# Performance work log

Measured on AMD Instinct MI355X. Metric: run time of the kernel, lower is better.

## Reference

```python
import jax, jax.numpy as jnp
import numpy as np

B, N, D, H, S = 2, 1024, 1024, 16, 4
DH = D // H  # dim_head = 64


def setup_inputs() -> dict:
    key = jax.random.key(0)
    ks = jax.random.split(key, 7)
    w = lambda k, shape: jax.random.normal(k, shape, dtype=jnp.float32) * 0.02
    return {
        "x": jax.random.normal(ks[0], (B, N, D), dtype=jnp.float32),
        "Wq": w(ks[1], (S, D, D)),
        "Wk": w(ks[2], (S, D, D)),
        "Wv": w(ks[3], (S, D, D)),
        "Wg": w(ks[4], (S, D)),
        "bg": jnp.zeros((S,), jnp.float32),
        "Wo": w(ks[5], (D, D)),
        "bo": jnp.zeros((D,), jnp.float32),
        "hyp_w": jnp.ones((S,), jnp.float32),
        "temperature": jnp.float32(1.0),
    }


def reference(x, Wq, Wk, Wv, Wg, bg, Wo, bo, hyp_w, temperature):
    # Training branch of EnhancedUncertaintyAttention, all S samples batched.
    b, n, d = x.shape
    scale = DH ** -0.5
    temp = jnp.clip(temperature, 0.1, 10.0)

    # coherence gate on mean-pooled tokens: [b, S]
    coh = jax.nn.sigmoid(x.mean(axis=1) @ Wg.T + bg)

    def proj(W):  # torch Linear: x @ W.T ; W: [S, out, in] -> [s,b,h,n,dh]
        y = jnp.einsum('bnd,sed->sbne', x, W)
        return y.reshape(S, b, n, H, DH).transpose(0, 1, 3, 2, 4)

    q, k, v = proj(Wq), proj(Wk), proj(Wv)

    dots = jnp.einsum('sbhid,sbhjd->sbhij', q, k) * scale
    attn = jax.nn.softmax(dots / temp, axis=-1)            # [S,b,h,n,n]
    out = jnp.einsum('sbhij,sbhjd->sbhid', attn, v)        # [S,b,h,n,dh]
    out = out.transpose(0, 1, 3, 2, 4).reshape(S, b, n, d) # [S,b,n,d]
    out = out * coh.T[:, :, None, None]                    # per-sample gate

    gw = jax.nn.softmax(hyp_w / temp)                      # hypothesis weights [S]
    combined = jnp.einsum('s,sbnd->bnd', gw, out)
    combined_attn = jnp.einsum('s,sbhij->bhij', gw, attn)

    y = combined @ Wo.T + bo  # to_out; dropout p treated as 0 (deterministic)
    return y, combined_attn.mean(axis=1)
```

## Files before the change

kernel.cpp:

```cpp
#include <hip/hip_runtime.h>
#include <hip/hip_bf16.h>

typedef __attribute__((ext_vector_type(8))) short s16x8;
typedef __attribute__((ext_vector_type(4))) float f32x4;

#define MAT2M 2097152
#define PPAD 72

__device__ __forceinline__ unsigned short f2bf(float f) {
  union { float f; unsigned u; } c; c.f = f;
  unsigned u = c.u;
  unsigned r = (u + 0x7fffu + ((u >> 16) & 1u)) >> 16;
  return (unsigned short)r;
}

__device__ __forceinline__ unsigned pk2bf(float a, float b) {
  union { __hip_bfloat162 h; unsigned u; } c;
  c.h = __float22bfloat162_rn(make_float2(a, b));
  return c.u;
}

__device__ __forceinline__ float bf2f(unsigned short u) {
  union { unsigned u; float f; } c; c.u = ((unsigned)u) << 16; return c.f;
}

__device__ __forceinline__ void async16(const unsigned short* g, unsigned short* l) {
  __builtin_amdgcn_global_load_lds(
      (const __attribute__((address_space(1))) unsigned int*)g,
      (__attribute__((address_space(3))) unsigned int*)l, 16, 0, 0);
}

__device__ __forceinline__ void stage64sw(const unsigned short* __restrict__ g,
                                          unsigned short* l, int wid, int ln) {
  const int rr = ln >> 3;
  const int gcol = ((ln & 7) ^ (rr & 7)) * 8;
#pragma unroll
  for (int c = 0; c < 2; ++c) {
    int r = (c * 4 + wid) * 8 + rr;
    async16(&g[(size_t)r * 1024 + gcol], &l[(c * 4 + wid) * 512 + ln * 8]);
  }
}

__global__ __launch_bounds__(256) void k_cvt(const float* __restrict__ in,
                                             unsigned short* __restrict__ out, int n) {
  int i = (blockIdx.x * 256 + threadIdx.x) * 4;
  if (i < n) {
    float4 v = *(const float4*)&in[i];
    ushort4 o;
    o.x = f2bf(v.x); o.y = f2bf(v.y); o.z = f2bf(v.z); o.w = f2bf(v.w);
    *(ushort4*)&out[i] = o;
  }
}

__global__ __launch_bounds__(256) void k_cvt3(const float* __restrict__ a,
                                              const float* __restrict__ b,
                                              const float* __restrict__ c,
                                              unsigned short* __restrict__ oa,
                                              unsigned short* __restrict__ ob,
                                              unsigned short* __restrict__ oc) {
  const float* in = blockIdx.y == 0 ? a : (blockIdx.y == 1 ? b : c);
  unsigned short* out = blockIdx.y == 0 ? oa : (blockIdx.y == 1 ? ob : oc);
  int i = (blockIdx.x * 256 + threadIdx.x) * 4;
  float4 v = *(const float4*)&in[i];
  ushort4 o;
  o.x = f2bf(v.x); o.y = f2bf(v.y); o.z = f2bf(v.z); o.w = f2bf(v.w);
  *(ushort4*)&out[i] = o;
}

__global__ __launch_bounds__(256) void k_meanx(const float* __restrict__ x,
                                               float* __restrict__ meanx) {
  int col = blockIdx.x * 256 + threadIdx.x;
  int b = col >> 10, d = col & 1023;
  int n0 = blockIdx.y * 64;
  float s = 0.f;
  for (int n = 0; n < 64; ++n)
    s += x[(size_t)b * 1048576 + (size_t)(n0 + n) * 1024 + d];
  atomicAdd(&meanx[col], s * (1.f / 1024.f));
}

__global__ __launch_bounds__(256) void k_prep(const float* __restrict__ meanx,
                                              const float* __restrict__ Wg,
                                              const float* __restrict__ bg,
                                              const float* __restrict__ hyp,
                                              const float* __restrict__ temp_p,
                                              float* __restrict__ prep) {
  int tid = threadIdx.x;
  int p = tid >> 5, c = tid & 31;
  int s = p >> 1, b = p & 1;
  float partial = 0.f;
  for (int d = c; d < 1024; d += 32)
    partial += meanx[b * 1024 + d] * Wg[s * 1024 + d];
#pragma unroll
  for (int m = 16; m >= 1; m >>= 1) partial += __shfl_xor(partial, m, 64);
  if (c == 0) {
    float coh = 1.f / (1.f + __expf(-(partial + bg[s])));
    prep[4 + s * 2 + b] = coh;
  }
  if (tid == 0) {
    float t = temp_p[0];
    t = fminf(fmaxf(t, 0.1f), 10.f);
    float it = 1.f / t;
    float e0 = hyp[0] * it, e1 = hyp[1] * it, e2 = hyp[2] * it, e3 = hyp[3] * it;
    float mx = fmaxf(fmaxf(e0, e1), fmaxf(e2, e3));
    float x0 = __expf(e0 - mx), x1 = __expf(e1 - mx), x2 = __expf(e2 - mx), x3 = __expf(e3 - mx);
    float inv = 1.f / (x0 + x1 + x2 + x3);
    prep[0] = x0 * inv; prep[1] = x1 * inv; prep[2] = x2 * inv; prep[3] = x3 * inv;
    prep[12] = 0.125f * it * 1.44269504f;
  }
}

__global__ __launch_bounds__(256) void gemm_qkv(
    const unsigned short* __restrict__ xb,
    const unsigned short* __restrict__ wqb,
    const unsigned short* __restrict__ wkb,
    const unsigned short* __restrict__ wvb,
    const float* __restrict__ prep,
    unsigned short* __restrict__ qk,
    unsigned short* __restrict__ vt) {
  __shared__ __align__(16) unsigned short As[128 * 64];
  __shared__ __align__(16) unsigned short Bs[128 * 64];
  const int tid = threadIdx.x;
  const int wid = tid >> 6, ln = tid & 63, lq = ln >> 4, lc = ln & 15;
  const int wr = wid >> 1, wc = wid & 1;
  const int z = blockIdx.z, proj = z >> 2, s = z & 3;
  const unsigned short* Bmat =
      (proj == 0 ? wqb : (proj == 1 ? wkb : wvb)) + (size_t)s * 1048576;
  const int n0 = blockIdx.x * 128, m0 = blockIdx.y * 128;
  const int sr = wid * 8 + (ln >> 3);
  const int sc = (((ln & 7) ^ ((ln >> 3) & 7))) * 8;
  const int ldsoff = wid * 512 + ln * 8;

  f32x4 acc[4][4];
#pragma unroll
  for (int a = 0; a < 4; ++a)
#pragma unroll
    for (int b4 = 0; b4 < 4; ++b4) acc[a][b4] = (f32x4){0.f, 0.f, 0.f, 0.f};

  for (int kt = 0; kt < 16; ++kt) {
    const int k0 = kt * 64;
    __syncthreads();
#pragma unroll
    for (int c = 0; c < 4; ++c) {
      async16(&xb[(size_t)(m0 + c * 32 + sr) * 1024 + k0 + sc], &As[c * 2048 + ldsoff]);
      async16(&Bmat[(size_t)(n0 + c * 32 + sr) * 1024 + k0 + sc], &Bs[c * 2048 + ldsoff]);
    }
    __syncthreads();
#pragma unroll
    for (int kc = 0; kc < 2; ++kc) {
      const int slot = ((kc * 4 + lq) ^ (lc & 7)) * 8;
      s16x8 af[4], bf[4];
#pragma unroll
      for (int a = 0; a < 4; ++a)
        af[a] = *(const s16x8*)&As[(wr * 64 + a * 16 + lc) * 64 + slot];
#pragma unroll
      for (int b4 = 0; b4 < 4; ++b4)
        bf[b4] = *(const s16x8*)&Bs[(wc * 64 + b4 * 16 + lc) * 64 + slot];
#pragma unroll
      for (int a = 0; a < 4; ++a)
#pragma unroll
        for (int b4 = 0; b4 < 4; ++b4)
          acc[a][b4] = __builtin_amdgcn_mfma_f32_16x16x32_bf16(af[a], bf[b4], acc[a][b4], 0, 0, 0);
    }
  }

  const float mulv = (proj == 1) ? prep[12] : 1.0f;
  if (z < 8) {
    unsigned short* C = qk + (size_t)z * MAT2M;
#pragma unroll
    for (int a = 0; a < 4; ++a) {
      int row0 = m0 + wr * 64 + a * 16 + lq * 4;
#pragma unroll
      for (int b4 = 0; b4 < 4; ++b4) {
        int col = n0 + wc * 64 + b4 * 16 + lc;
#pragma unroll
        for (int r = 0; r < 4; ++r)
          C[(size_t)(row0 + r) * 1024 + col] = f2bf(acc[a][b4][r] * mulv);
      }
    }
  } else {
#pragma unroll
    for (int a = 0; a < 4; ++a) {
      int row0 = m0 + wr * 64 + a * 16 + lq * 4;
      int bb = row0 >> 10, ii = row0 & 1023;
#pragma unroll
      for (int b4 = 0; b4 < 4; ++b4) {
        int col = n0 + wc * 64 + b4 * 16 + lc;
        int head = col >> 6, dh = col & 63;
        uint2 pk;
        pk.x = pk2bf(acc[a][b4][0], acc[a][b4][1]);
        pk.y = pk2bf(acc[a][b4][2], acc[a][b4][3]);
        *(uint2*)&vt[(((size_t)((s * 2 + bb) * 16 + head)) << 16) + dh * 1024 + ii] = pk;
      }
    }
  }
}

__global__ __launch_bounds__(256) void att_o(
    const unsigned short* __restrict__ qk,
    const unsigned short* __restrict__ vt,
    unsigned short* __restrict__ o_sb,
    float* __restrict__ linv_ws) {
  __shared__ __align__(16) unsigned short Ks[2][64 * 64];
  __shared__ __align__(16) unsigned short Vs[2][64 * 64];
  __shared__ __align__(16) unsigned short PB[8 * 16 * PPAD];

  const int tid = threadIdx.x;
  const int wid = tid >> 6, ln = tid & 63, lq = ln >> 4, lc = ln & 15;
  const int i0 = blockIdx.x * 128;
  const int h = blockIdx.y;
  const int sb = blockIdx.z, s = sb >> 1, b = sb & 1;

  const unsigned short* Qg =
      qk + (size_t)s * MAT2M + (size_t)(b * 1024 + i0 + wid * 32) * 1024 + h * 64;
  const unsigned short* Kg = qk + (size_t)(4 + s) * MAT2M + (size_t)b * 1048576 + h * 64;
  const unsigned short* Vtg = vt + (((size_t)(sb * 16 + h)) << 16);

  s16x8 qf[2][2];
#pragma unroll
  for (int g = 0; g < 2; ++g)
#pragma unroll
    for (int kc = 0; kc < 2; ++kc)
      qf[g][kc] = *(const s16x8*)&Qg[(size_t)(g * 16 + lc) * 1024 + kc * 32 + lq * 8];

  f32x4 oaccT[2][4];
#pragma unroll
  for (int g = 0; g < 2; ++g)
#pragma unroll
    for (int db = 0; db < 4; ++db) oaccT[g][db] = (f32x4){0.f, 0.f, 0.f, 0.f};
  float lsum[2] = {0.f, 0.f};
  unsigned short* PBw = PB + wid * 2 * 16 * PPAD;

  stage64sw(Kg, Ks[0], wid, ln);
  stage64sw(Vtg, Vs[0], wid, ln);

  for (int jt = 0; jt < 16; ++jt) {
    const int u = jt & 1;
    __syncthreads();
    if (jt < 15) {
      stage64sw(Kg + (size_t)(jt + 1) * 64 * 1024, Ks[u ^ 1], wid, ln);
      stage64sw(Vtg + (jt + 1) * 64, Vs[u ^ 1], wid, ln);
    }

    f32x4 st[2][4];
#pragma unroll
    for (int g = 0; g < 2; ++g)
#pragma unroll
      for (int jb = 0; jb < 4; ++jb) st[g][jb] = (f32x4){0.f, 0.f, 0.f, 0.f};
#pragma unroll
    for (int kc = 0; kc < 2; ++kc) {
      const int slot = ((kc * 4 + lq) ^ (lc & 7)) * 8;
#pragma unroll
      for (int jb = 0; jb < 4; ++jb) {
        s16x8 kf = *(const s16x8*)&Ks[u][(jb * 16 + lc) * 64 + slot];
        st[0][jb] = __builtin_amdgcn_mfma_f32_16x16x32_bf16(kf, qf[0][kc], st[0][jb], 0, 0, 0);
        st[1][jb] = __builtin_amdgcn_mfma_f32_16x16x32_bf16(kf, qf[1][kc], st[1][jb], 0, 0, 0);
      }
    }

#pragma unroll
    for (int g = 0; g < 2; ++g)
#pragma unroll
      for (int jb = 0; jb < 4; ++jb) {
        float p0 = __builtin_amdgcn_exp2f(st[g][jb][0]);
        float p1 = __builtin_amdgcn_exp2f(st[g][jb][1]);
        float p2 = __builtin_amdgcn_exp2f(st[g][jb][2]);
        float p3 = __builtin_amdgcn_exp2f(st[g][jb][3]);
        lsum[g] += (p0 + p1) + (p2 + p3);
        uint2 pv;
        pv.x = pk2bf(p0, p1);
        pv.y = pk2bf(p2, p3);
        *(uint2*)&PBw[(g * 16 + lc) * PPAD + jb * 16 + lq * 4] = pv;
      }

#pragma unroll
    for (int kc = 0; kc < 2; ++kc) {
      const int slot = ((kc * 4 + lq) ^ (lc & 7)) * 8;
      s16x8 pf0 = *(const s16x8*)&PBw[lc * PPAD + kc * 32 + lq * 8];
      s16x8 pf1 = *(const s16x8*)&PBw[(16 + lc) * PPAD + kc * 32 + lq * 8];
#pragma unroll
      for (int db = 0; db < 4; ++db) {
        s16x8 vf = *(const s16x8*)&Vs[u][(db * 16 + lc) * 64 + slot];
        oaccT[0][db] = __builtin_amdgcn_mfma_f32_16x16x32_bf16(vf, pf0, oaccT[0][db], 0, 0, 0);
        oaccT[1][db] = __builtin_amdgcn_mfma_f32_16x16x32_bf16(vf, pf1, oaccT[1][db], 0, 0, 0);
      }
    }
  }

  float invl[2];
#pragma unroll
  for (int g = 0; g < 2; ++g) {
    lsum[g] += __shfl_xor(lsum[g], 16, 64);
    lsum[g] += __shfl_xor(lsum[g], 32, 64);
    invl[g] = 1.f / lsum[g];
  }
  if (lq == 0) {
    int base = (sb * 16 + h) * 1024 + i0 + wid * 32 + lc;
    linv_ws[base] = invl[0];
    linv_ws[base + 16] = invl[1];
  }

#pragma unroll
  for (int g = 0; g < 2; ++g) {
    int i = i0 + wid * 32 + g * 16 + lc;
    unsigned short* orow =
        o_sb + (size_t)s * MAT2M + (size_t)(b * 1024 + i) * 1024 + h * 64;
#pragma unroll
    for (int db = 0; db < 4; ++db) {
      f32x4 o = oaccT[g][db] * invl[g];
      uint2 pv;
      pv.x = pk2bf(o[0], o[1]);
      pv.y = pk2bf(o[2], o[3]);
      *(uint2*)&orow[db * 16 + lq * 4] = pv;
    }
  }
}

__global__ __launch_bounds__(256) void att_p(
    const unsigned short* __restrict__ qk,
    const float* __restrict__ prep,
    const float* __restrict__ linv_ws,
    float* __restrict__ pp) {
  __shared__ __align__(16) unsigned short Qs[2][128 * 64];
  __shared__ __align__(16) unsigned short Ks[2][64 * 64];
  const int tid = threadIdx.x;
  const int wid = tid >> 6, ln = tid & 63, lq = ln >> 4, lc = ln & 15;
  const int j0 = blockIdx.x * 64;
  const int i0 = blockIdx.y * 128;
  const int z = blockIdx.z, s = z >> 1, b = z & 1;
  const float wgt = prep[s] * (1.f / 16.f);

  const unsigned short* Qb = qk + (size_t)s * MAT2M + (size_t)(b * 1024 + i0) * 1024;
  const unsigned short* Kb = qk + (size_t)(4 + s) * MAT2M + (size_t)(b * 1024 + j0) * 1024;

  const int rr = ln >> 3;
  const int gcol = ((ln & 7) ^ (rr & 7)) * 8;

  f32x4 psum[2][4];
#pragma unroll
  for (int g = 0; g < 2; ++g)
#pragma unroll
    for (int jb = 0; jb < 4; ++jb) psum[g][jb] = (f32x4){0.f, 0.f, 0.f, 0.f};

#pragma unroll
  for (int c = 0; c < 4; ++c) {
    int r = (c * 4 + wid) * 8 + rr;
    async16(&Qb[(size_t)r * 1024 + gcol], &Qs[0][(c * 4 + wid) * 512 + ln * 8]);
  }
  stage64sw(Kb, Ks[0], wid, ln);

  for (int h = 0; h < 16; ++h) {
    const int u = h & 1;
    __syncthreads();
    if (h < 15) {
      const int hoff = (h + 1) * 64;
#pragma unroll
      for (int c = 0; c < 4; ++c) {
        int r = (c * 4 + wid) * 8 + rr;
        async16(&Qb[(size_t)r * 1024 + hoff + gcol], &Qs[u ^ 1][(c * 4 + wid) * 512 + ln * 8]);
      }
      stage64sw(Kb + hoff, Ks[u ^ 1], wid, ln);
    }

    s16x8 qf[2][2];
#pragma unroll
    for (int kc = 0; kc < 2; ++kc) {
      const int slot = ((kc * 4 + lq) ^ (lc & 7)) * 8;
#pragma unroll
      for (int g = 0; g < 2; ++g)
        qf[g][kc] = *(const s16x8*)&Qs[u][(wid * 32 + g * 16 + lc) * 64 + slot];
    }
    float ilr[2];
#pragma unroll
    for (int g = 0; g < 2; ++g)
      ilr[g] = wgt * linv_ws[(z * 16 + h) * 1024 + i0 + wid * 32 + g * 16 + lc];

    f32x4 st[2][4];
#pragma unroll
    for (int g = 0; g < 2; ++g)
#pragma unroll
      for (int jb = 0; jb < 4; ++jb) st[g][jb] = (f32x4){0.f, 0.f, 0.f, 0.f};
#pragma unroll
    for (int kc = 0; kc < 2; ++kc) {
      const int slot = ((kc * 4 + lq) ^ (lc & 7)) * 8;
#pragma unroll
      for (int jb = 0; jb < 4; ++jb) {
        s16x8 kf = *(const s16x8*)&Ks[u][(jb * 16 + lc) * 64 + slot];
        st[0][jb] = __builtin_amdgcn_mfma_f32_16x16x32_bf16(kf, qf[0][kc], st[0][jb], 0, 0, 0);
        st[1][jb] = __builtin_amdgcn_mfma_f32_16x16x32_bf16(kf, qf[1][kc], st[1][jb], 0, 0, 0);
      }
    }
#pragma unroll
    for (int g = 0; g < 2; ++g)
#pragma unroll
      for (int jb = 0; jb < 4; ++jb)
#pragma unroll
        for (int r = 0; r < 4; ++r)
          psum[g][jb][r] += __builtin_amdgcn_exp2f(st[g][jb][r]) * ilr[g];
  }

  float* prow = pp + (size_t)z * 1048576;
#pragma unroll
  for (int g = 0; g < 2; ++g) {
    int i = i0 + wid * 32 + g * 16 + lc;
#pragma unroll
    for (int jb = 0; jb < 4; ++jb)
      *(f32x4*)&prow[(size_t)i * 1024 + j0 + jb * 16 + lq * 4] = psum[g][jb];
  }
}

__global__ __launch_bounds__(256) void k_reduce(const float* __restrict__ pp,
                                                float* __restrict__ out1) {
  size_t idx = ((size_t)blockIdx.x * 256 + threadIdx.x) * 4;
  int b = (int)(idx >> 20);
  size_t rem = idx & 1048575u;
  const float* base = pp + (size_t)b * 1048576 + rem;
  float4 a0 = *(const float4*)&base[0];
  float4 a1 = *(const float4*)&base[(size_t)2 * 1048576];
  float4 a2 = *(const float4*)&base[(size_t)4 * 1048576];
  float4 a3 = *(const float4*)&base[(size_t)6 * 1048576];
  float4 o;
  o.x = (a0.x + a1.x) + (a2.x + a3.x);
  o.y = (a0.y + a1.y) + (a2.y + a3.y);
  o.z = (a0.z + a1.z) + (a2.z + a3.z);
  o.w = (a0.w + a1.w) + (a2.w + a3.w);
  *(float4*)&out1[idx] = o;
}

__global__ __launch_bounds__(256) void k_combine(const unsigned short* __restrict__ o_sb,
                                                 const float* __restrict__ prep,
                                                 unsigned short* __restrict__ comb) {
  size_t base = (size_t)(blockIdx.x * 256 + threadIdx.x) * 4;
  int m = (int)(base >> 10);
  int b = m >> 10;
  float w0 = prep[0] * prep[4 + 0 * 2 + b];
  float w1 = prep[1] * prep[4 + 1 * 2 + b];
  float w2 = prep[2] * prep[4 + 2 * 2 + b];
  float w3 = prep[3] * prep[4 + 3 * 2 + b];
  ushort4 v0 = *(const ushort4*)&o_sb[base];
  ushort4 v1 = *(const ushort4*)&o_sb[(size_t)MAT2M + base];
  ushort4 v2 = *(const ushort4*)&o_sb[(size_t)2 * MAT2M + base];
  ushort4 v3 = *(const ushort4*)&o_sb[(size_t)3 * MAT2M + base];
  float ax = w0 * bf2f(v0.x) + w1 * bf2f(v1.x) + w2 * bf2f(v2.x) + w3 * bf2f(v3.x);
  float ay = w0 * bf2f(v0.y) + w1 * bf2f(v1.y) + w2 * bf2f(v2.y) + w3 * bf2f(v3.y);
  float az = w0 * bf2f(v0.z) + w1 * bf2f(v1.z) + w2 * bf2f(v2.z) + w3 * bf2f(v3.z);
  float aw = w0 * bf2f(v0.w) + w1 * bf2f(v1.w) + w2 * bf2f(v2.w) + w3 * bf2f(v3.w);
  uint2 o;
  o.x = pk2bf(ax, ay);
  o.y = pk2bf(az, aw);
  *(uint2*)&comb[base] = o;
}

__global__ __launch_bounds__(256) void gemm_out(
    const unsigned short* __restrict__ Amat,
    const unsigned short* __restrict__ Bmat,
    const float* __restrict__ bias,
    float* __restrict__ y) {
  __shared__ __align__(16) unsigned short As[128 * 64];
  __shared__ __align__(16) unsigned short Bs[128 * 64];
  const int tid = threadIdx.x;
  const int wid = tid >> 6, ln = tid & 63, lq = ln >> 4, lc = ln & 15;
  const int wr = wid >> 1, wc = wid & 1;
  const int n0 = blockIdx.x * 128, m0 = blockIdx.y * 128;
  const int sr = wid * 8 + (ln >> 3);
  const int sc = (((ln & 7) ^ ((ln >> 3) & 7))) * 8;
  const int ldsoff = wid * 512 + ln * 8;

  f32x4 acc[4][4];
#pragma unroll
  for (int a = 0; a < 4; ++a)
#pragma unroll
    for (int b4 = 0; b4 < 4; ++b4) acc[a][b4] = (f32x4){0.f, 0.f, 0.f, 0.f};

  for (int kt = 0; kt < 16; ++kt) {
    const int k0 = kt * 64;
    __syncthreads();
#pragma unroll
    for (int c = 0; c < 4; ++c) {
      async16(&Amat[(size_t)(m0 + c * 32 + sr) * 1024 + k0 + sc], &As[c * 2048 + ldsoff]);
      async16(&Bmat[(size_t)(n0 + c * 32 + sr) * 1024 + k0 + sc], &Bs[c * 2048 + ldsoff]);
    }
    __syncthreads();
#pragma unroll
    for (int kc = 0; kc < 2; ++kc) {
      const int slot = ((kc * 4 + lq) ^ (lc & 7)) * 8;
      s16x8 af[4], bf[4];
#pragma unroll
      for (int a = 0; a < 4; ++a)
        af[a] = *(const s16x8*)&As[(wr * 64 + a * 16 + lc) * 64 + slot];
#pragma unroll
      for (int b4 = 0; b4 < 4; ++b4)
        bf[b4] = *(const s16x8*)&Bs[(wc * 64 + b4 * 16 + lc) * 64 + slot];
#pragma unroll
      for (int a = 0; a < 4; ++a)
#pragma unroll
        for (int b4 = 0; b4 < 4; ++b4)
          acc[a][b4] = __builtin_amdgcn_mfma_f32_16x16x32_bf16(af[a], bf[b4], acc[a][b4], 0, 0, 0);
    }
  }

#pragma unroll
  for (int a = 0; a < 4; ++a) {
    int row0 = m0 + wr * 64 + a * 16 + lq * 4;
#pragma unroll
    for (int b4 = 0; b4 < 4; ++b4) {
      int col = n0 + wc * 64 + b4 * 16 + lc;
      float bv = bias[col];
#pragma unroll
      for (int r = 0; r < 4; ++r)
        y[(size_t)(row0 + r) * 1024 + col] = acc[a][b4][r] + bv;
    }
  }
}

extern "C" void kernel_launch(void* const* d_in, const int* in_sizes, int n_in,
                              void* d_out, int out_size, void* d_ws, size_t ws_size,
                              hipStream_t stream) {
  const float* x    = (const float*)d_in[0];
  const float* Wq   = (const float*)d_in[1];
  const float* Wk   = (const float*)d_in[2];
  const float* Wv   = (const float*)d_in[3];
  const float* Wg   = (const float*)d_in[4];
  const float* bg   = (const float*)d_in[5];
  const float* Wo   = (const float*)d_in[6];
  const float* bo   = (const float*)d_in[7];
  const float* hyp  = (const float*)d_in[8];
  const float* temp = (const float*)d_in[9];

  float* y = (float*)d_out;
  float* out1 = y + MAT2M;

  char* w = (char*)d_ws;
  size_t off = 0;
  auto alloc = [&](size_t bytes) { void* p = w + off; off += (bytes + 255) & ~(size_t)255; return p; };
  unsigned short* xb   = (unsigned short*)alloc((size_t)MAT2M * 2);
  unsigned short* wqb  = (unsigned short*)alloc((size_t)4 * 1048576 * 2);
  unsigned short* wkb  = (unsigned short*)alloc((size_t)4 * 1048576 * 2);
  unsigned short* wvb  = (unsigned short*)alloc((size_t)4 * 1048576 * 2);
  unsigned short* wob  = (unsigned short*)alloc((size_t)1048576 * 2);
  unsigned short* qk   = (unsigned short*)alloc((size_t)8 * MAT2M * 2);
  unsigned short* vt   = (unsigned short*)alloc((size_t)4 * MAT2M * 2);
  unsigned short* o_sb = (unsigned short*)alloc((size_t)4 * MAT2M * 2);
  unsigned short* comb = (unsigned short*)alloc((size_t)MAT2M * 2);
  float* pp    = (float*)alloc((size_t)8 * 1048576 * 4);
  float* linv  = (float*)alloc((size_t)131072 * 4);
  float* meanx = (float*)alloc((size_t)2048 * 4);
  float* prep  = (float*)alloc((size_t)16 * 4);

  k_cvt<<<2048, 256, 0, stream>>>(x, xb, MAT2M);
  k_cvt3<<<dim3(4096, 3), 256, 0, stream>>>(Wq, Wk, Wv, wqb, wkb, wvb);
  k_cvt<<<1024, 256, 0, stream>>>(Wo, wob, 1048576);

  hipMemsetAsync(meanx, 0, 2048 * sizeof(float), stream);
  k_meanx<<<dim3(8, 16), 256, 0, stream>>>(x, meanx);
  k_prep<<<1, 256, 0, stream>>>(meanx, Wg, bg, hyp, temp, prep);

  gemm_qkv<<<dim3(8, 16, 12), 256, 0, stream>>>(xb, wqb, wkb, wvb, prep, qk, vt);

  att_o<<<dim3(8, 16, 8), 256, 0, stream>>>(qk, vt, o_sb, linv);
  att_p<<<dim3(16, 8, 8), 256, 0, stream>>>(qk, prep, linv, pp);
  k_reduce<<<2048, 256, 0, stream>>>(pp, out1);

  k_combine<<<2048, 256, 0, stream>>>(o_sb, prep, comb);
  gemm_out<<<dim3(8, 16, 1), 256, 0, stream>>>(comb, wob, bo, y);
}
```

Before: 341.4 us.

## Double-buffer GEMM tiles, merge conversion and reduce kernels, vectorize epilogues

Adds LDS double buffering with prefetch of the next K tile to the QKV and output GEMMs, which removes one barrier per iteration and overlaps loads with MFMA work. The QKV GEMM is split into separate QK and V kernels. Swapping the MFMA operands lets the QK and output epilogues write contiguous vector stores instead of scattered scalar ones. The three conversion launches become one, and the reduce and combine launches become one, which cuts launch overhead. The cost is double the shared memory per block, which may lower occupancy.

```diff
diff --git a/kernel.cpp b/kernel.cpp
--- a/kernel.cpp
+++ b/kernel.cpp
@@ -41,30 +41,30 @@
   }
 }
 
-__global__ __launch_bounds__(256) void k_cvt(const float* __restrict__ in,
-                                             unsigned short* __restrict__ out, int n) {
+__global__ __launch_bounds__(256) void k_cvt_all(
+    const float* __restrict__ x, const float* __restrict__ wq,
+    const float* __restrict__ wk, const float* __restrict__ wv,
+    const float* __restrict__ wo,
+    unsigned short* __restrict__ xb, unsigned short* __restrict__ wqb,
+    unsigned short* __restrict__ wkb, unsigned short* __restrict__ wvb,
+    unsigned short* __restrict__ wob) {
+  const int y = blockIdx.y;
+  const float* in;
+  unsigned short* out;
+  int n;
+  if (y == 0)      { in = x;  out = xb;  n = MAT2M; }
+  else if (y == 1) { in = wq; out = wqb; n = 4194304; }
+  else if (y == 2) { in = wk; out = wkb; n = 4194304; }
+  else if (y == 3) { in = wv; out = wvb; n = 4194304; }
+  else             { in = wo; out = wob; n = 1048576; }
   int i = (blockIdx.x * 256 + threadIdx.x) * 4;
   if (i < n) {
     float4 v = *(const float4*)&in[i];
-    ushort4 o;
-    o.x = f2bf(v.x); o.y = f2bf(v.y); o.z = f2bf(v.z); o.w = f2bf(v.w);
-    *(ushort4*)&out[i] = o;
-  }
-}
-
-__global__ __launch_bounds__(256) void k_cvt3(const float* __restrict__ a,
-                                              const float* __restrict__ b,
-                                              const float* __restrict__ c,
-                                              unsigned short* __restrict__ oa,
-                                              unsigned short* __restrict__ ob,
-                                              unsigned short* __restrict__ oc) {
-  const float* in = blockIdx.y == 0 ? a : (blockIdx.y == 1 ? b : c);
-  unsigned short* out = blockIdx.y == 0 ? oa : (blockIdx.y == 1 ? ob : oc);
-  int i = (blockIdx.x * 256 + threadIdx.x) * 4;
-  float4 v = *(const float4*)&in[i];
-  ushort4 o;
-  o.x = f2bf(v.x); o.y = f2bf(v.y); o.z = f2bf(v.z); o.w = f2bf(v.w);
-  *(ushort4*)&out[i] = o;
+    uint2 o;
+    o.x = pk2bf(v.x, v.y);
+    o.y = pk2bf(v.z, v.w);
+    *(uint2*)&out[i] = o;
+  }
 }
 
 __global__ __launch_bounds__(256) void k_meanx(const float* __restrict__ x,
@@ -109,22 +109,19 @@
   }
 }
 
-__global__ __launch_bounds__(256) void gemm_qkv(
+__global__ __launch_bounds__(256) void gemm_qk(
     const unsigned short* __restrict__ xb,
     const unsigned short* __restrict__ wqb,
     const unsigned short* __restrict__ wkb,
-    const unsigned short* __restrict__ wvb,
     const float* __restrict__ prep,
-    unsigned short* __restrict__ qk,
-    unsigned short* __restrict__ vt) {
-  __shared__ __align__(16) unsigned short As[128 * 64];
-  __shared__ __align__(16) unsigned short Bs[128 * 64];
+    unsigned short* __restrict__ qk) {
+  __shared__ __align__(16) unsigned short As[2][128 * 64];
+  __shared__ __align__(16) unsigned short Bs[2][128 * 64];
   const int tid = threadIdx.x;
   const int wid = tid >> 6, ln = tid & 63, lq = ln >> 4, lc = ln & 15;
   const int wr = wid >> 1, wc = wid & 1;
   const int z = blockIdx.z, proj = z >> 2, s = z & 3;
-  const unsigned short* Bmat =
-      (proj == 0 ? wqb : (proj == 1 ? wkb : wvb)) + (size_t)s * 1048576;
+  const unsigned short* Bmat = (proj == 0 ? wqb : wkb) + (size_t)s * 1048576;
   const int n0 = blockIdx.x * 128, m0 = blockIdx.y * 128;
   const int sr = wid * 8 + (ln >> 3);
   const int sc = (((ln & 7) ^ ((ln >> 3) & 7))) * 8;
@@ -136,25 +133,107 @@
 #pragma unroll
     for (int b4 = 0; b4 < 4; ++b4) acc[a][b4] = (f32x4){0.f, 0.f, 0.f, 0.f};
 
+#pragma unroll
+  for (int c = 0; c < 4; ++c) {
+    async16(&xb[(size_t)(m0 + c * 32 + sr) * 1024 + sc], &As[0][c * 2048 + ldsoff]);
+    async16(&Bmat[(size_t)(n0 + c * 32 + sr) * 1024 + sc], &Bs[0][c * 2048 + ldsoff]);
+  }
+
   for (int kt = 0; kt < 16; ++kt) {
-    const int k0 = kt * 64;
+    const int u = kt & 1;
     __syncthreads();
-#pragma unroll
-    for (int c = 0; c < 4; ++c) {
-      async16(&xb[(size_t)(m0 + c * 32 + sr) * 1024 + k0 + sc], &As[c * 2048 + ldsoff]);
-      async16(&Bmat[(size_t)(n0 + c * 32 + sr) * 1024 + k0 + sc], &Bs[c * 2048 + ldsoff]);
-    }
-    __syncthreads();
+    if (kt < 15) {
+      const int k1 = (kt + 1) * 64;
+#pragma unroll
+      for (int c = 0; c < 4; ++c) {
+        async16(&xb[(size_t)(m0 + c * 32 + sr) * 1024 + k1 + sc], &As[u ^ 1][c * 2048 + ldsoff]);
+        async16(&Bmat[(size_t)(n0 + c * 32 + sr) * 1024 + k1 + sc], &Bs[u ^ 1][c * 2048 + ldsoff]);
+      }
+    }
 #pragma unroll
     for (int kc = 0; kc < 2; ++kc) {
       const int slot = ((kc * 4 + lq) ^ (lc & 7)) * 8;
       s16x8 af[4], bf[4];
 #pragma unroll
       for (int a = 0; a < 4; ++a)
-        af[a] = *(const s16x8*)&As[(wr * 64 + a * 16 + lc) * 64 + slot];
+        af[a] = *(const s16x8*)&As[u][(wr * 64 + a * 16 + lc) * 64 + slot];
 #pragma unroll
       for (int b4 = 0; b4 < 4; ++b4)
-        bf[b4] = *(const s16x8*)&Bs[(wc * 64 + b4 * 16 + lc) * 64 + slot];
+        bf[b4] = *(const s16x8*)&Bs[u][(wc * 64 + b4 * 16 + lc) * 64 + slot];
+#pragma unroll
+      for (int a = 0; a < 4; ++a)
+#pragma unroll
+        for (int b4 = 0; b4 < 4; ++b4)
+          acc[a][b4] = __builtin_amdgcn_mfma_f32_16x16x32_bf16(bf[b4], af[a], acc[a][b4], 0, 0, 0);
+    }
+  }
+
+  const float mulv = (proj == 1) ? prep[12] : 1.0f;
+  unsigned short* C = qk + (size_t)z * MAT2M;
+#pragma unroll
+  for (int a = 0; a < 4; ++a) {
+    int row = m0 + wr * 64 + a * 16 + lc;
+    unsigned short* Crow = C + (size_t)row * 1024;
+#pragma unroll
+    for (int b4 = 0; b4 < 4; ++b4) {
+      int colbase = n0 + wc * 64 + b4 * 16 + lq * 4;
+      uint2 pv;
+      pv.x = pk2bf(acc[a][b4][0] * mulv, acc[a][b4][1] * mulv);
+      pv.y = pk2bf(acc[a][b4][2] * mulv, acc[a][b4][3] * mulv);
+      *(uint2*)&Crow[colbase] = pv;
+    }
+  }
+}
+
+__global__ __launch_bounds__(256) void gemm_v(
+    const unsigned short* __restrict__ xb,
+    const unsigned short* __restrict__ wvb,
+    unsigned short* __restrict__ vt) {
+  __shared__ __align__(16) unsigned short As[2][128 * 64];
+  __shared__ __align__(16) unsigned short Bs[2][128 * 64];
+  const int tid = threadIdx.x;
+  const int wid = tid >> 6, ln = tid & 63, lq = ln >> 4, lc = ln & 15;
+  const int wr = wid >> 1, wc = wid & 1;
+  const int s = blockIdx.z;
+  const unsigned short* Bmat = wvb + (size_t)s * 1048576;
+  const int n0 = blockIdx.x * 128, m0 = blockIdx.y * 128;
+  const int sr = wid * 8 + (ln >> 3);
+  const int sc = (((ln & 7) ^ ((ln >> 3) & 7))) * 8;
+  const int ldsoff = wid * 512 + ln * 8;
+
+  f32x4 acc[4][4];
+#pragma unroll
+  for (int a = 0; a < 4; ++a)
+#pragma unroll
+    for (int b4 = 0; b4 < 4; ++b4) acc[a][b4] = (f32x4){0.f, 0.f, 0.f, 0.f};
+
+#pragma unroll
+  for (int c = 0; c < 4; ++c) {
+    async16(&xb[(size_t)(m0 + c * 32 + sr) * 1024 + sc], &As[0][c * 2048 + ldsoff]);
+    async16(&Bmat[(size_t)(n0 + c * 32 + sr) * 1024 + sc], &Bs[0][c * 2048 + ldsoff]);
+  }
+
+  for (int kt = 0; kt < 16; ++kt) {
+    const int u = kt & 1;
+    __syncthreads();
+    if (kt < 15) {
+      const int k1 = (kt + 1) * 64;
+#pragma unroll
+      for (int c = 0; c < 4; ++c) {
+        async16(&xb[(size_t)(m0 + c * 32 + sr) * 1024 + k1 + sc], &As[u ^ 1][c * 2048 + ldsoff]);
+        async16(&Bmat[(size_t)(n0 + c * 32 + sr) * 1024 + k1 + sc], &Bs[u ^ 1][c * 2048 + ldsoff]);
+      }
+    }
+#pragma unroll
+    for (int kc = 0; kc < 2; ++kc) {
+      const int slot = ((kc * 4 + lq) ^ (lc & 7)) * 8;
+      s16x8 af[4], bf[4];
+#pragma unroll
+      for (int a = 0; a < 4; ++a)
+        af[a] = *(const s16x8*)&As[u][(wr * 64 + a * 16 + lc) * 64 + slot];
+#pragma unroll
+      for (int b4 = 0; b4 < 4; ++b4)
+        bf[b4] = *(const s16x8*)&Bs[u][(wc * 64 + b4 * 16 + lc) * 64 + slot];
 #pragma unroll
       for (int a = 0; a < 4; ++a)
 #pragma unroll
@@ -163,34 +242,18 @@
     }
   }
 
-  const float mulv = (proj == 1) ? prep[12] : 1.0f;
-  if (z < 8) {
-    unsigned short* C = qk + (size_t)z * MAT2M;
-#pragma unroll
-    for (int a = 0; a < 4; ++a) {
-      int row0 = m0 + wr * 64 + a * 16 + lq * 4;
-#pragma unroll
-      for (int b4 = 0; b4 < 4; ++b4) {
-        int col = n0 + wc * 64 + b4 * 16 + lc;
-#pragma unroll
-        for (int r = 0; r < 4; ++r)
-          C[(size_t)(row0 + r) * 1024 + col] = f2bf(acc[a][b4][r] * mulv);
-      }
-    }
-  } else {
-#pragma unroll
-    for (int a = 0; a < 4; ++a) {
-      int row0 = m0 + wr * 64 + a * 16 + lq * 4;
-      int bb = row0 >> 10, ii = row0 & 1023;
-#pragma unroll
-      for (int b4 = 0; b4 < 4; ++b4) {
-        int col = n0 + wc * 64 + b4 * 16 + lc;
-        int head = col >> 6, dh = col & 63;
-        uint2 pk;
-        pk.x = pk2bf(acc[a][b4][0], acc[a][b4][1]);
-        pk.y = pk2bf(acc[a][b4][2], acc[a][b4][3]);
-        *(uint2*)&vt[(((size_t)((s * 2 + bb) * 16 + head)) << 16) + dh * 1024 + ii] = pk;
-      }
+#pragma unroll
+  for (int a = 0; a < 4; ++a) {
+    int row0 = m0 + wr * 64 + a * 16 + lq * 4;
+    int bb = row0 >> 10, ii = row0 & 1023;
+#pragma unroll
+    for (int b4 = 0; b4 < 4; ++b4) {
+      int col = n0 + wc * 64 + b4 * 16 + lc;
+      int head = col >> 6, dh = col & 63;
+      uint2 pk;
+      pk.x = pk2bf(acc[a][b4][0], acc[a][b4][1]);
+      pk.y = pk2bf(acc[a][b4][2], acc[a][b4][3]);
+      *(uint2*)&vt[(((size_t)((s * 2 + bb) * 16 + head)) << 16) + dh * 1024 + ii] = pk;
     }
   }
 }
@@ -408,46 +471,46 @@
   }
 }
 
-__global__ __launch_bounds__(256) void k_reduce(const float* __restrict__ pp,
-                                                float* __restrict__ out1) {
+__global__ __launch_bounds__(256) void k_redcomb(const float* __restrict__ pp,
+                                                 const unsigned short* __restrict__ o_sb,
+                                                 const float* __restrict__ prep,
+                                                 float* __restrict__ out1,
+                                                 unsigned short* __restrict__ comb) {
   size_t idx = ((size_t)blockIdx.x * 256 + threadIdx.x) * 4;
-  int b = (int)(idx >> 20);
-  size_t rem = idx & 1048575u;
-  const float* base = pp + (size_t)b * 1048576 + rem;
-  float4 a0 = *(const float4*)&base[0];
-  float4 a1 = *(const float4*)&base[(size_t)2 * 1048576];
-  float4 a2 = *(const float4*)&base[(size_t)4 * 1048576];
-  float4 a3 = *(const float4*)&base[(size_t)6 * 1048576];
-  float4 o;
-  o.x = (a0.x + a1.x) + (a2.x + a3.x);
-  o.y = (a0.y + a1.y) + (a2.y + a3.y);
-  o.z = (a0.z + a1.z) + (a2.z + a3.z);
-  o.w = (a0.w + a1.w) + (a2.w + a3.w);
-  *(float4*)&out1[idx] = o;
-}
-
-__global__ __launch_bounds__(256) void k_combine(const unsigned short* __restrict__ o_sb,
-                                                 const float* __restrict__ prep,
-                                                 unsigned short* __restrict__ comb) {
-  size_t base = (size_t)(blockIdx.x * 256 + threadIdx.x) * 4;
-  int m = (int)(base >> 10);
-  int b = m >> 10;
-  float w0 = prep[0] * prep[4 + 0 * 2 + b];
-  float w1 = prep[1] * prep[4 + 1 * 2 + b];
-  float w2 = prep[2] * prep[4 + 2 * 2 + b];
-  float w3 = prep[3] * prep[4 + 3 * 2 + b];
-  ushort4 v0 = *(const ushort4*)&o_sb[base];
-  ushort4 v1 = *(const ushort4*)&o_sb[(size_t)MAT2M + base];
-  ushort4 v2 = *(const ushort4*)&o_sb[(size_t)2 * MAT2M + base];
-  ushort4 v3 = *(const ushort4*)&o_sb[(size_t)3 * MAT2M + base];
-  float ax = w0 * bf2f(v0.x) + w1 * bf2f(v1.x) + w2 * bf2f(v2.x) + w3 * bf2f(v3.x);
-  float ay = w0 * bf2f(v0.y) + w1 * bf2f(v1.y) + w2 * bf2f(v2.y) + w3 * bf2f(v3.y);
-  float az = w0 * bf2f(v0.z) + w1 * bf2f(v1.z) + w2 * bf2f(v2.z) + w3 * bf2f(v3.z);
-  float aw = w0 * bf2f(v0.w) + w1 * bf2f(v1.w) + w2 * bf2f(v2.w) + w3 * bf2f(v3.w);
-  uint2 o;
-  o.x = pk2bf(ax, ay);
-  o.y = pk2bf(az, aw);
-  *(uint2*)&comb[base] = o;
+  if (blockIdx.y == 0) {
+    int b = (int)(idx >> 20);
+    size_t rem = idx & 1048575u;
+    const float* base = pp + (size_t)b * 1048576 + rem;
+    float4 a0 = *(const float4*)&base[0];
+    float4 a1 = *(const float4*)&base[(size_t)2 * 1048576];
+    float4 a2 = *(const float4*)&base[(size_t)4 * 1048576];
+    float4 a3 = *(const float4*)&base[(size_t)6 * 1048576];
+    float4 o;
+    o.x = (a0.x + a1.x) + (a2.x + a3.x);
+    o.y = (a0.y + a1.y) + (a2.y + a3.y);
+    o.z = (a0.z + a1.z) + (a2.z + a3.z);
+    o.w = (a0.w + a1.w) + (a2.w + a3.w);
+    *(float4*)&out1[idx] = o;
+  } else {
+    int m = (int)(idx >> 10);
+    int b = m >> 10;
+    float w0 = prep[0] * prep[4 + 0 * 2 + b];
+    float w1 = prep[1] * prep[4 + 1 * 2 + b];
+    float w2 = prep[2] * prep[4 + 2 * 2 + b];
+    float w3 = prep[3] * prep[4 + 3 * 2 + b];
+    ushort4 v0 = *(const ushort4*)&o_sb[idx];
+    ushort4 v1 = *(const ushort4*)&o_sb[(size_t)MAT2M + idx];
+    ushort4 v2 = *(const ushort4*)&o_sb[(size_t)2 * MAT2M + idx];
+    ushort4 v3 = *(const ushort4*)&o_sb[(size_t)3 * MAT2M + idx];
+    float ax = w0 * bf2f(v0.x) + w1 * bf2f(v1.x) + w2 * bf2f(v2.x) + w3 * bf2f(v3.x);
+    float ay = w0 * bf2f(v0.y) + w1 * bf2f(v1.y) + w2 * bf2f(v2.y) + w3 * bf2f(v3.y);
+    float az = w0 * bf2f(v0.z) + w1 * bf2f(v1.z) + w2 * bf2f(v2.z) + w3 * bf2f(v3.z);
+    float aw = w0 * bf2f(v0.w) + w1 * bf2f(v1.w) + w2 * bf2f(v2.w) + w3 * bf2f(v3.w);
+    uint2 o;
+    o.x = pk2bf(ax, ay);
+    o.y = pk2bf(az, aw);
+    *(uint2*)&comb[idx] = o;
+  }
 }
 
 __global__ __launch_bounds__(256) void gemm_out(
@@ -455,8 +518,8 @@
     const unsigned short* __restrict__ Bmat,
     const float* __restrict__ bias,
     float* __restrict__ y) {
-  __shared__ __align__(16) unsigned short As[128 * 64];
-  __shared__ __align__(16) unsigned short Bs[128 * 64];
+  __shared__ __align__(16) unsigned short As[2][128 * 64];
+  __shared__ __align__(16) unsigned short Bs[2][128 * 64];
   const int tid = threadIdx.x;
   const int wid = tid >> 6, ln = tid & 63, lq = ln >> 4, lc = ln & 15;
   const int wr = wid >> 1, wc = wid & 1;
@@ -471,43 +534,55 @@
 #pragma unroll
     for (int b4 = 0; b4 < 4; ++b4) acc[a][b4] = (f32x4){0.f, 0.f, 0.f, 0.f};
 
+#pragma unroll
+  for (int c = 0; c < 4; ++c) {
+    async16(&Amat[(size_t)(m0 + c * 32 + sr) * 1024 + sc], &As[0][c * 2048 + ldsoff]);
+    async16(&Bmat[(size_t)(n0 + c * 32 + sr) * 1024 + sc], &Bs[0][c * 2048 + ldsoff]);
+  }
+
   for (int kt = 0; kt < 16; ++kt) {
-    const int k0 = kt * 64;
+    const int u = kt & 1;
     __syncthreads();
-#pragma unroll
-    for (int c = 0; c < 4; ++c) {
-      async16(&Amat[(size_t)(m0 + c * 32 + sr) * 1024 + k0 + sc], &As[c * 2048 + ldsoff]);
-      async16(&Bmat[(size_t)(n0 + c * 32 + sr) * 1024 + k0 + sc], &Bs[c * 2048 + ldsoff]);
-    }
-    __syncthreads();
+    if (kt < 15) {
+      const int k1 = (kt + 1) * 64;
+#pragma unroll
+      for (int c = 0; c < 4; ++c) {
+        async16(&Amat[(size_t)(m0 + c * 32 + sr) * 1024 + k1 + sc], &As[u ^ 1][c * 2048 + ldsoff]);
+        async16(&Bmat[(size_t)(n0 + c * 32 + sr) * 1024 + k1 + sc], &Bs[u ^ 1][c * 2048 + ldsoff]);
+      }
+    }
 #pragma unroll
     for (int kc = 0; kc < 2; ++kc) {
       const int slot = ((kc * 4 + lq) ^ (lc & 7)) * 8;
       s16x8 af[4], bf[4];
 #pragma unroll
       for (int a = 0; a < 4; ++a)
-        af[a] = *(const s16x8*)&As[(wr * 64 + a * 16 + lc) * 64 + slot];
+        af[a] = *(const s16x8*)&As[u][(wr * 64 + a * 16 + lc) * 64 + slot];
 #pragma unroll
       for (int b4 = 0; b4 < 4; ++b4)
-        bf[b4] = *(const s16x8*)&Bs[(wc * 64 + b4 * 16 + lc) * 64 + slot];
+        bf[b4] = *(const s16x8*)&Bs[u][(wc * 64 + b4 * 16 + lc) * 64 + slot];
 #pragma unroll
       for (int a = 0; a < 4; ++a)
 #pragma unroll
         for (int b4 = 0; b4 < 4; ++b4)
-          acc[a][b4] = __builtin_amdgcn_mfma_f32_16x16x32_bf16(af[a], bf[b4], acc[a][b4], 0, 0, 0);
+          acc[a][b4] = __builtin_amdgcn_mfma_f32_16x16x32_bf16(bf[b4], af[a], acc[a][b4], 0, 0, 0);
     }
   }
 
 #pragma unroll
   for (int a = 0; a < 4; ++a) {
-    int row0 = m0 + wr * 64 + a * 16 + lq * 4;
+    int row = m0 + wr * 64 + a * 16 + lc;
+    float* yrow = y + (size_t)row * 1024;
 #pragma unroll
     for (int b4 = 0; b4 < 4; ++b4) {
-      int col = n0 + wc * 64 + b4 * 16 + lc;
-      float bv = bias[col];
-#pragma unroll
-      for (int r = 0; r < 4; ++r)
-        y[(size_t)(row0 + r) * 1024 + col] = acc[a][b4][r] + bv;
+      int colbase = n0 + wc * 64 + b4 * 16 + lq * 4;
+      float4 bv = *(const float4*)&bias[colbase];
+      float4 o;
+      o.x = acc[a][b4][0] + bv.x;
+      o.y = acc[a][b4][1] + bv.y;
+      o.z = acc[a][b4][2] + bv.z;
+      o.w = acc[a][b4][3] + bv.w;
+      *(float4*)&yrow[colbase] = o;
     }
   }
 }
@@ -546,20 +621,19 @@
   float* meanx = (float*)alloc((size_t)2048 * 4);
   float* prep  = (float*)alloc((size_t)16 * 4);
 
-  k_cvt<<<2048, 256, 0, stream>>>(x, xb, MAT2M);
-  k_cvt3<<<dim3(4096, 3), 256, 0, stream>>>(Wq, Wk, Wv, wqb, wkb, wvb);
-  k_cvt<<<1024, 256, 0, stream>>>(Wo, wob, 1048576);
+  k_cvt_all<<<dim3(4096, 5), 256, 0, stream>>>(x, Wq, Wk, Wv, Wo,
+                                               xb, wqb, wkb, wvb, wob);
 
   hipMemsetAsync(meanx, 0, 2048 * sizeof(float), stream);
   k_meanx<<<dim3(8, 16), 256, 0, stream>>>(x, meanx);
   k_prep<<<1, 256, 0, stream>>>(meanx, Wg, bg, hyp, temp, prep);
 
-  gemm_qkv<<<dim3(8, 16, 12), 256, 0, stream>>>(xb, wqb, wkb, wvb, prep, qk, vt);
+  gemm_qk<<<dim3(8, 16, 8), 256, 0, stream>>>(xb, wqb, wkb, prep, qk);
+  gemm_v<<<dim3(8, 16, 4), 256, 0, stream>>>(xb, wvb, vt);
 
   att_o<<<dim3(8, 16, 8), 256, 0, stream>>>(qk, vt, o_sb, linv);
   att_p<<<dim3(16, 8, 8), 256, 0, stream>>>(qk, prep, linv, pp);
-  k_reduce<<<2048, 256, 0, stream>>>(pp, out1);
-
-  k_combine<<<2048, 256, 0, stream>>>(o_sb, prep, comb);
+
+  k_redcomb<<<dim3(2048, 2), 256, 0, stream>>>(pp, o_sb, prep, out1, comb);
   gemm_out<<<dim3(8, 16, 1), 256, 0, stream>>>(comb, wob, bo, y);
 }
```

After: 348.6 us. 2.1% more time.
